# Kernel tuning notes

Hardware: AMD Instinct MI355X
Metric: run time of the kernel (lower is better)

Reference implementation:

```python
import jax, jax.numpy as jnp
import numpy as np

N_IN, N_RES, N_OUT = 64, 2048, 64
B, T = 32, 1024
SPECTRAL_RADIUS = 0.9
DENSITY = 0.1


def setup_inputs() -> dict:
    key = jax.random.key(0)
    k_x, k_in, k_res, k_mask, k_br, k_wo, k_bo = jax.random.split(key, 7)
    x = jax.random.normal(k_x, (B, T, N_IN), dtype=jnp.float32)
    W_in = jax.random.normal(k_in, (N_RES, N_IN), dtype=jnp.float32) * 0.1
    # Sparse random reservoir, rescaled to approximate spectral radius.
    W_dense = jax.random.normal(k_res, (N_RES, N_RES), dtype=jnp.float32)
    mask = (jax.random.uniform(k_mask, (N_RES, N_RES)) < DENSITY).astype(jnp.float32)
    W_sp = W_dense * mask
    # circular law: spectral radius of sparse gaussian ~ sqrt(N * density)
    W_res = W_sp * (SPECTRAL_RADIUS / jnp.sqrt(N_RES * DENSITY))
    b_res = jax.random.normal(k_br, (N_RES,), dtype=jnp.float32) * 0.01
    W_out = jax.random.normal(k_wo, (N_OUT, N_RES), dtype=jnp.float32) * 0.02
    b_out = jax.random.normal(k_bo, (N_OUT,), dtype=jnp.float32) * 0.01
    return {"x": x, "W_in": W_in, "W_res": W_res, "b_res": b_res,
            "W_out": W_out, "b_out": b_out}


def reference(x, W_in, W_res, b_res, W_out, b_out):
    # Precompute input projections for all timesteps: [B,T,N_RES]
    xin = jnp.einsum('btd,nd->btn', x, W_in) + b_res
    xin_t = jnp.transpose(xin, (1, 0, 2))  # [T,B,N]

    def step(h, u_t):
        # h: [B,N]; u_t: [B,N] precomputed W_in x_t + b
        h_new = jnp.tanh(u_t + h @ W_res.T)
        return h_new, h_new

    h0 = jnp.zeros((x.shape[0], W_res.shape[0]), dtype=x.dtype)
    _, states_t = jax.lax.scan(step, h0, xin_t)  # [T,B,N]
    states = jnp.transpose(states_t, (1, 0, 2))  # [B,T,N]
    # Linear readout (CustomReadoutLayer with activation_fn=None)
    y = jnp.einsum('btn,on->bto', states, W_out) + b_out  # [B,T,N_OUT]
    return y
```

## Files before the change

kernel.cpp:

```cpp
#include <hip/hip_runtime.h>
#include <stdint.h>

#define NRES 2048
#define NIN  64
#define NOUT 64
#define BB   32
#define TT   1024

typedef __attribute__((ext_vector_type(8))) short bf16x8;
typedef __attribute__((ext_vector_type(4))) float f32x4;

__device__ __forceinline__ float bf2f(uint16_t u) {
  union { uint32_t i; float f; } v; v.i = ((uint32_t)u) << 16; return v.f;
}
__device__ __forceinline__ uint16_t f2bf_rne(float f) {
  union { float f; uint32_t i; } v; v.f = f;
  uint32_t lsb = (v.i >> 16) & 1u;
  v.i += 0x7fffu + lsb;
  return (uint16_t)(v.i >> 16);
}
__device__ __forceinline__ short hi16(float f) {
  return (short)(__float_as_uint(f) >> 16);
}
__device__ __forceinline__ bf16x8 pack8(float4 a, float4 b) {
  bf16x8 r;
  r[0] = hi16(a.x); r[1] = hi16(a.y); r[2] = hi16(a.z); r[3] = hi16(a.w);
  r[4] = hi16(b.x); r[5] = hi16(b.y); r[6] = hi16(b.z); r[7] = hi16(b.w);
  return r;
}

__global__ __launch_bounds__(256) void esn_init(const float* __restrict__ b_out,
                                                float* __restrict__ y,
                                                uint32_t* __restrict__ hz) {
  int idx = blockIdx.x * 256 + threadIdx.x;
  y[idx] = b_out[idx & 63];
  if (idx < 65536) hz[idx] = 0u;
}

__global__ __launch_bounds__(512) void esn_step(
    const float* __restrict__ x,
    const float* __restrict__ W_in,
    const float* __restrict__ W_res,
    const float* __restrict__ b_res,
    const float* __restrict__ W_out,
    const uint16_t* __restrict__ h_hi,
    const uint16_t* __restrict__ h_lo,
    uint16_t* __restrict__ ho_hi,
    uint16_t* __restrict__ ho_lo,
    float* __restrict__ y,
    int t)
{
  __shared__ float wos[NOUT][17];
  __shared__ float red[8][16][17];
  __shared__ float hs[16][17];

  int tid   = threadIdx.x;
  int l     = tid & 63;
  int w     = tid >> 6;
  int btile = blockIdx.x & 1;
  int r0    = (blockIdx.x >> 1) << 4;
  int m16   = l & 15;
  int kg    = l >> 4;

  if (tid < 256) {
    int o = tid >> 2, jj = (tid & 3) * 4;
    float4 wv = *reinterpret_cast<const float4*>(W_out + (size_t)o * NRES + r0 + jj);
    wos[o][jj + 0] = wv.x; wos[o][jj + 1] = wv.y;
    wos[o][jj + 2] = wv.z; wos[o][jj + 3] = wv.w;
  }

  int b = btile * 16 + m16;
  f32x4 acc = {0.f, 0.f, 0.f, 0.f};

  const float*    ap = W_res + (size_t)(r0 + m16) * NRES + w * 256 + kg * 8;
  const uint16_t* bh = h_hi + (size_t)b * NRES + w * 256 + kg * 8;
  const uint16_t* bl = h_lo + (size_t)b * NRES + w * 256 + kg * 8;
#pragma unroll
  for (int c = 0; c < 8; ++c) {
    float4 a0 = *reinterpret_cast<const float4*>(ap);
    float4 a1 = *reinterpret_cast<const float4*>(ap + 4);
    bf16x8 af  = pack8(a0, a1);
    bf16x8 bh8 = *reinterpret_cast<const bf16x8*>(bh);
    bf16x8 bl8 = *reinterpret_cast<const bf16x8*>(bl);
    acc = __builtin_amdgcn_mfma_f32_16x16x32_bf16(af, bh8, acc, 0, 0, 0);
    acc = __builtin_amdgcn_mfma_f32_16x16x32_bf16(af, bl8, acc, 0, 0, 0);
    ap += 32; bh += 32; bl += 32;
  }

  if (w == 0) {
    const float* aip = W_in + (size_t)(r0 + m16) * NIN + kg * 8;
    const float* xp  = x + (size_t)b * (TT * NIN) + (size_t)t * NIN + kg * 8;
#pragma unroll
    for (int c = 0; c < 2; ++c) {
      float4 a0 = *reinterpret_cast<const float4*>(aip);
      float4 a1 = *reinterpret_cast<const float4*>(aip + 4);
      float4 x0 = *reinterpret_cast<const float4*>(xp);
      float4 x1 = *reinterpret_cast<const float4*>(xp + 4);
      acc = __builtin_amdgcn_mfma_f32_16x16x32_bf16(pack8(a0, a1), pack8(x0, x1), acc, 0, 0, 0);
      aip += 32; xp += 32;
    }
  }

#pragma unroll
  for (int j = 0; j < 4; ++j) red[w][kg * 4 + j][m16] = acc[j];
  __syncthreads();

  if (tid < 256) {
    int rowM = tid & 15, colB = tid >> 4;
    float s = b_res[r0 + rowM];
#pragma unroll
    for (int ww = 0; ww < 8; ++ww) s += red[ww][rowM][colB];
    float h = tanhf(s);
    uint16_t hh = f2bf_rne(h);
    float rem = h - bf2f(hh);
    uint16_t hl = f2bf_rne(rem);
    int bg = btile * 16 + colB;
    ho_hi[(size_t)bg * NRES + r0 + rowM] = hh;
    ho_lo[(size_t)bg * NRES + r0 + rowM] = hl;
    hs[rowM][colB] = h;
  }
  __syncthreads();

#pragma unroll
  for (int q = 0; q < 2; ++q) {
    int p = tid * 2 + q;
    int o = p >> 4, colB = p & 15;
    float d = 0.f;
#pragma unroll
    for (int rm = 0; rm < 16; ++rm) d += wos[o][rm] * hs[rm][colB];
    atomicAdd(y + (size_t)(btile * 16 + colB) * (TT * NOUT) + (size_t)t * NOUT + o, d);
  }
}

__global__ __launch_bounds__(256) void legacy_init(const float* __restrict__ b_out,
                                                   float* __restrict__ y,
                                                   float* __restrict__ h0) {
  int idx = blockIdx.x * 256 + threadIdx.x;
  y[idx] = b_out[idx & 63];
  if (idx < NRES * BB) h0[idx] = 0.0f;
}

__global__ __launch_bounds__(256) void legacy_step(
    const float* __restrict__ x, const float* __restrict__ W_in,
    const float* __restrict__ W_res, const float* __restrict__ b_res,
    const float* __restrict__ W_out, const float* __restrict__ h_in,
    float* __restrict__ h_out, float* __restrict__ y, int t)
{
  __shared__ float xs[BB][NIN + 1];
  __shared__ float hsL[8][BB + 1];
  __shared__ float wosL[NOUT][9];
  int tid = threadIdx.x;
  int r0  = blockIdx.x << 3;
  {
    int i = tid * 8, b = i >> 6, d = i & 63;
    const float* src = x + (size_t)b * (TT * NIN) + (size_t)t * NIN + d;
    float4 v0 = *reinterpret_cast<const float4*>(src);
    float4 v1 = *reinterpret_cast<const float4*>(src + 4);
    xs[b][d + 0] = v0.x; xs[b][d + 1] = v0.y; xs[b][d + 2] = v0.z; xs[b][d + 3] = v0.w;
    xs[b][d + 4] = v1.x; xs[b][d + 5] = v1.y; xs[b][d + 6] = v1.z; xs[b][d + 7] = v1.w;
  }
  {
    int o = tid >> 2, jj = (tid & 3) * 2;
    float2 w2 = *reinterpret_cast<const float2*>(W_out + (size_t)o * NRES + r0 + jj);
    wosL[o][jj] = w2.x; wosL[o][jj + 1] = w2.y;
  }
  __syncthreads();
  int b = tid & 31, rr = tid >> 5, r = r0 + rr;
  float acc = b_res[r];
  const float* wi = W_in + (size_t)r * NIN;
#pragma unroll
  for (int d = 0; d < NIN; d += 8) {
    float4 w0 = *reinterpret_cast<const float4*>(wi + d);
    float4 w1 = *reinterpret_cast<const float4*>(wi + d + 4);
    acc += w0.x * xs[b][d + 0] + w0.y * xs[b][d + 1] + w0.z * xs[b][d + 2] + w0.w * xs[b][d + 3] +
           w1.x * xs[b][d + 4] + w1.y * xs[b][d + 5] + w1.z * xs[b][d + 6] + w1.w * xs[b][d + 7];
  }
  const float* wr = W_res + (size_t)r * NRES;
  const float* hbp = h_in + b;
  for (int k = 0; k < NRES; k += 8) {
    float4 w0 = *reinterpret_cast<const float4*>(wr + k);
    float4 w1 = *reinterpret_cast<const float4*>(wr + k + 4);
    acc += w0.x * hbp[(size_t)(k + 0) * BB] + w0.y * hbp[(size_t)(k + 1) * BB] +
           w0.z * hbp[(size_t)(k + 2) * BB] + w0.w * hbp[(size_t)(k + 3) * BB] +
           w1.x * hbp[(size_t)(k + 4) * BB] + w1.y * hbp[(size_t)(k + 5) * BB] +
           w1.z * hbp[(size_t)(k + 6) * BB] + w1.w * hbp[(size_t)(k + 7) * BB];
  }
  float h = tanhf(acc);
  h_out[r * BB + b] = h;
  hsL[rr][b] = h;
  __syncthreads();
  float h8[8];
#pragma unroll
  for (int j = 0; j < 8; ++j) h8[j] = hsL[j][b];
  float* yrow = y + (size_t)b * (TT * NOUT) + (size_t)t * NOUT;
#pragma unroll
  for (int oo = 0; oo < 8; ++oo) {
    int o = oo * 8 + rr;
    float p = 0.f;
#pragma unroll
    for (int j = 0; j < 8; ++j) p += h8[j] * wosL[o][j];
    atomicAdd(yrow + o, p);
  }
}

extern "C" void kernel_launch(void* const* d_in, const int* in_sizes, int n_in,
                              void* d_out, int out_size, void* d_ws, size_t ws_size,
                              hipStream_t stream) {
  const float* p_x = 0; const float* p_Win = 0; const float* p_Wres = 0;
  const float* p_bres = 0; const float* p_Wout = 0; const float* p_bout = 0;
  for (int i = 0; i < n_in; ++i) {
    const float* p = (const float*)d_in[i];
    switch (in_sizes[i]) {
      case 2097152: p_x = p; break;
      case 4194304: p_Wres = p; break;
      case 2048:    p_bres = p; break;
      case 64:      p_bout = p; break;
      case 131072:  if (!p_Win) p_Win = p; else p_Wout = p; break;
      default: break;
    }
  }
  if (!p_x || !p_Win || !p_Wres || !p_bres || !p_Wout || !p_bout) {
    p_x    = (const float*)d_in[0];
    p_Win  = (const float*)d_in[1];
    p_Wres = (const float*)d_in[2];
    p_bres = (const float*)d_in[3];
    p_Wout = (const float*)d_in[4];
    p_bout = (const float*)d_in[5];
  }

  float* y = (float*)d_out;

  if (ws_size >= 524288) {
    uint16_t* hA_hi = (uint16_t*)d_ws;
    uint16_t* hA_lo = (uint16_t*)((char*)d_ws + 131072);
    uint16_t* hB_hi = (uint16_t*)((char*)d_ws + 262144);
    uint16_t* hB_lo = (uint16_t*)((char*)d_ws + 393216);

    esn_init<<<dim3(8192), dim3(256), 0, stream>>>(p_bout, y, (uint32_t*)d_ws);

    uint16_t *ihi = hA_hi, *ilo = hA_lo, *ohi = hB_hi, *olo = hB_lo;
    for (int t = 0; t < TT; ++t) {
      esn_step<<<dim3(256), dim3(512), 0, stream>>>(p_x, p_Win, p_Wres, p_bres, p_Wout,
                                                    ihi, ilo, ohi, olo, y, t);
      uint16_t* s;
      s = ihi; ihi = ohi; ohi = s;
      s = ilo; ilo = olo; olo = s;
    }
  } else {
    float* h0 = (float*)d_ws;
    float* h1 = (float*)((char*)d_ws + 262144);
    legacy_init<<<dim3(8192), dim3(256), 0, stream>>>(p_bout, y, h0);
    float* ha = h0; float* hb = h1;
    for (int t = 0; t < TT; ++t) {
      legacy_step<<<dim3(256), dim3(256), 0, stream>>>(p_x, p_Win, p_Wres, p_bres, p_Wout,
                                                       ha, hb, y, t);
      float* tmp = ha; ha = hb; hb = tmp;
    }
  }
}
```

Measured before the change: 17.13 ms.

## Cover both batch tiles per block to reuse W_res rows, halve grid

Each block now computes 16 reservoir rows for all 32 batch entries instead of 16, so the W_res tile is loaded and converted to bf16 once per block rather than twice across two blocks. The grid shrinks from 256 to 128 blocks, and W_res loads are hoisted ahead of the MFMA loop with split accumulators to increase instruction-level parallelism. This halves W_res global traffic per step but uses fewer blocks, which reduces parallelism on a GPU with many CUs and raises register pressure.

```diff
diff --git a/kernel.cpp b/kernel.cpp
--- a/kernel.cpp
+++ b/kernel.cpp
@@ -51,61 +51,88 @@
     int t)
 {
   __shared__ float wos[NOUT][17];
-  __shared__ float red[8][16][17];
-  __shared__ float hs[16][17];
-
-  int tid   = threadIdx.x;
-  int l     = tid & 63;
-  int w     = tid >> 6;
-  int btile = blockIdx.x & 1;
-  int r0    = (blockIdx.x >> 1) << 4;
-  int m16   = l & 15;
-  int kg    = l >> 4;
-
-  if (tid < 256) {
-    int o = tid >> 2, jj = (tid & 3) * 4;
-    float4 wv = *reinterpret_cast<const float4*>(W_out + (size_t)o * NRES + r0 + jj);
-    wos[o][jj + 0] = wv.x; wos[o][jj + 1] = wv.y;
-    wos[o][jj + 2] = wv.z; wos[o][jj + 3] = wv.w;
-  }
-
-  int b = btile * 16 + m16;
-  f32x4 acc = {0.f, 0.f, 0.f, 0.f};
-
-  const float*    ap = W_res + (size_t)(r0 + m16) * NRES + w * 256 + kg * 8;
-  const uint16_t* bh = h_hi + (size_t)b * NRES + w * 256 + kg * 8;
-  const uint16_t* bl = h_lo + (size_t)b * NRES + w * 256 + kg * 8;
+  __shared__ float red[8][16][33];
+  __shared__ float hs[16][33];
+
+  int tid = threadIdx.x;
+  int l   = tid & 63;
+  int w   = tid >> 6;
+  int r0  = blockIdx.x << 4;
+  int m16 = l & 15;
+  int kg  = l >> 4;
+
+  {
+    int o = tid >> 3, jj = (tid & 7) * 2;
+    float2 w2 = *reinterpret_cast<const float2*>(W_out + (size_t)o * NRES + r0 + jj);
+    wos[o][jj] = w2.x; wos[o][jj + 1] = w2.y;
+  }
+
+  f32x4 acc00 = {0.f,0.f,0.f,0.f};
+  f32x4 acc01 = {0.f,0.f,0.f,0.f};
+  f32x4 acc10 = {0.f,0.f,0.f,0.f};
+  f32x4 acc11 = {0.f,0.f,0.f,0.f};
+
+  const float* ap = W_res + (size_t)(r0 + m16) * NRES + w * 256 + kg * 8;
+  float4 w4a[8], w4b[8];
 #pragma unroll
   for (int c = 0; c < 8; ++c) {
-    float4 a0 = *reinterpret_cast<const float4*>(ap);
-    float4 a1 = *reinterpret_cast<const float4*>(ap + 4);
-    bf16x8 af  = pack8(a0, a1);
-    bf16x8 bh8 = *reinterpret_cast<const bf16x8*>(bh);
-    bf16x8 bl8 = *reinterpret_cast<const bf16x8*>(bl);
-    acc = __builtin_amdgcn_mfma_f32_16x16x32_bf16(af, bh8, acc, 0, 0, 0);
-    acc = __builtin_amdgcn_mfma_f32_16x16x32_bf16(af, bl8, acc, 0, 0, 0);
-    ap += 32; bh += 32; bl += 32;
+    w4a[c] = *reinterpret_cast<const float4*>(ap + c * 32);
+    w4b[c] = *reinterpret_cast<const float4*>(ap + c * 32 + 4);
+  }
+
+  const uint16_t* hb0 = h_hi + (size_t)m16 * NRES        + w * 256 + kg * 8;
+  const uint16_t* hb1 = h_hi + (size_t)(16 + m16) * NRES + w * 256 + kg * 8;
+  const uint16_t* lb0 = h_lo + (size_t)m16 * NRES        + w * 256 + kg * 8;
+  const uint16_t* lb1 = h_lo + (size_t)(16 + m16) * NRES + w * 256 + kg * 8;
+
+#pragma unroll
+  for (int c = 0; c < 8; ++c) {
+    bf16x8 af = pack8(w4a[c], w4b[c]);
+    bf16x8 h0 = *reinterpret_cast<const bf16x8*>(hb0 + c * 32);
+    bf16x8 h1 = *reinterpret_cast<const bf16x8*>(hb1 + c * 32);
+    bf16x8 l0 = *reinterpret_cast<const bf16x8*>(lb0 + c * 32);
+    bf16x8 l1 = *reinterpret_cast<const bf16x8*>(lb1 + c * 32);
+    if (c < 4) {
+      acc00 = __builtin_amdgcn_mfma_f32_16x16x32_bf16(af, h0, acc00, 0, 0, 0);
+      acc00 = __builtin_amdgcn_mfma_f32_16x16x32_bf16(af, l0, acc00, 0, 0, 0);
+      acc01 = __builtin_amdgcn_mfma_f32_16x16x32_bf16(af, h1, acc01, 0, 0, 0);
+      acc01 = __builtin_amdgcn_mfma_f32_16x16x32_bf16(af, l1, acc01, 0, 0, 0);
+    } else {
+      acc10 = __builtin_amdgcn_mfma_f32_16x16x32_bf16(af, h0, acc10, 0, 0, 0);
+      acc10 = __builtin_amdgcn_mfma_f32_16x16x32_bf16(af, l0, acc10, 0, 0, 0);
+      acc11 = __builtin_amdgcn_mfma_f32_16x16x32_bf16(af, h1, acc11, 0, 0, 0);
+      acc11 = __builtin_amdgcn_mfma_f32_16x16x32_bf16(af, l1, acc11, 0, 0, 0);
+    }
   }
 
   if (w == 0) {
     const float* aip = W_in + (size_t)(r0 + m16) * NIN + kg * 8;
-    const float* xp  = x + (size_t)b * (TT * NIN) + (size_t)t * NIN + kg * 8;
 #pragma unroll
     for (int c = 0; c < 2; ++c) {
-      float4 a0 = *reinterpret_cast<const float4*>(aip);
-      float4 a1 = *reinterpret_cast<const float4*>(aip + 4);
-      float4 x0 = *reinterpret_cast<const float4*>(xp);
-      float4 x1 = *reinterpret_cast<const float4*>(xp + 4);
-      acc = __builtin_amdgcn_mfma_f32_16x16x32_bf16(pack8(a0, a1), pack8(x0, x1), acc, 0, 0, 0);
-      aip += 32; xp += 32;
-    }
-  }
-
-#pragma unroll
-  for (int j = 0; j < 4; ++j) red[w][kg * 4 + j][m16] = acc[j];
-  __syncthreads();
-
-  if (tid < 256) {
+      float4 a0 = *reinterpret_cast<const float4*>(aip + c * 32);
+      float4 a1 = *reinterpret_cast<const float4*>(aip + c * 32 + 4);
+      bf16x8 af = pack8(a0, a1);
+      const float* xp0 = x + (size_t)m16 * (TT * NIN)        + (size_t)t * NIN + c * 32 + kg * 8;
+      const float* xp1 = x + (size_t)(16 + m16) * (TT * NIN) + (size_t)t * NIN + c * 32 + kg * 8;
+      bf16x8 xb0 = pack8(*reinterpret_cast<const float4*>(xp0),
+                         *reinterpret_cast<const float4*>(xp0 + 4));
+      bf16x8 xb1 = pack8(*reinterpret_cast<const float4*>(xp1),
+                         *reinterpret_cast<const float4*>(xp1 + 4));
+      acc00 = __builtin_amdgcn_mfma_f32_16x16x32_bf16(af, xb0, acc00, 0, 0, 0);
+      acc01 = __builtin_amdgcn_mfma_f32_16x16x32_bf16(af, xb1, acc01, 0, 0, 0);
+    }
+  }
+
+  f32x4 s0 = acc00 + acc10;
+  f32x4 s1 = acc01 + acc11;
+#pragma unroll
+  for (int j = 0; j < 4; ++j) {
+    red[w][kg * 4 + j][m16]      = s0[j];
+    red[w][kg * 4 + j][16 + m16] = s1[j];
+  }
+  __syncthreads();
+
+  {
     int rowM = tid & 15, colB = tid >> 4;
     float s = b_res[r0 + rowM];
 #pragma unroll
@@ -113,22 +140,20 @@
     float h = tanhf(s);
     uint16_t hh = f2bf_rne(h);
     float rem = h - bf2f(hh);
-    uint16_t hl = f2bf_rne(rem);
-    int bg = btile * 16 + colB;
-    ho_hi[(size_t)bg * NRES + r0 + rowM] = hh;
-    ho_lo[(size_t)bg * NRES + r0 + rowM] = hl;
+    ho_hi[(size_t)colB * NRES + r0 + rowM] = hh;
+    ho_lo[(size_t)colB * NRES + r0 + rowM] = f2bf_rne(rem);
     hs[rowM][colB] = h;
   }
   __syncthreads();
 
 #pragma unroll
-  for (int q = 0; q < 2; ++q) {
-    int p = tid * 2 + q;
-    int o = p >> 4, colB = p & 15;
+  for (int q = 0; q < 4; ++q) {
+    int p = tid * 4 + q;
+    int o = p >> 5, b = p & 31;
     float d = 0.f;
 #pragma unroll
-    for (int rm = 0; rm < 16; ++rm) d += wos[o][rm] * hs[rm][colB];
-    atomicAdd(y + (size_t)(btile * 16 + colB) * (TT * NOUT) + (size_t)t * NOUT + o, d);
+    for (int rm = 0; rm < 16; ++rm) d += wos[o][rm] * hs[rm][b];
+    atomicAdd(y + (size_t)b * (TT * NOUT) + (size_t)t * NOUT + o, d);
   }
 }
 
@@ -240,7 +265,7 @@
 
     uint16_t *ihi = hA_hi, *ilo = hA_lo, *ohi = hB_hi, *olo = hB_lo;
     for (int t = 0; t < TT; ++t) {
-      esn_step<<<dim3(256), dim3(512), 0, stream>>>(p_x, p_Win, p_Wres, p_bres, p_Wout,
+      esn_step<<<dim3(128), dim3(512), 0, stream>>>(p_x, p_Win, p_Wres, p_bres, p_Wout,
                                                     ihi, ilo, ohi, olo, y, t);
       uint16_t* s;
       s = ihi; ihi = ohi; ohi = s;
```

After: 23.49 ms. 37.1% more time.
